# Kernel tuning notes

Measured on AMD Instinct MI355X. Metric: run time of the kernel, lower is better.

Reference implementation:

```python
import jax, jax.numpy as jnp
import numpy as np

NODE_DIM, EDGE_DIM, HIDDEN = 64, 16, 128
B, N, E, EA = 4, 10000, 320000, 80000


def _lin(key, fan_in, fan_out):
    # xavier-uniform like torch init
    bound = (6.0 / (fan_in + fan_out)) ** 0.5
    w = jax.random.uniform(key, (fan_in, fan_out), jnp.float32, -bound, bound)
    b = jnp.zeros((fan_out,), jnp.float32)
    return w, b


def setup_inputs() -> dict:
    key = jax.random.key(0)
    ks = jax.random.split(key, 12)
    nodes = jax.random.normal(ks[0], (B, N, NODE_DIM), jnp.float32)
    edge_index = jax.random.randint(ks[1], (2, E), 0, N, jnp.int64)
    edge_attr = jax.random.normal(ks[2], (B, E, EDGE_DIM), jnp.float32)
    edge_type_mask = jax.random.randint(ks[3], (EA,), 0, E, jnp.int64)
    p = {}
    p['g1_mw1'], p['g1_mb1'] = _lin(ks[4], 2 * NODE_DIM + EDGE_DIM, HIDDEN)
    p['g1_mw2'], p['g1_mb2'] = _lin(ks[5], HIDDEN, HIDDEN)
    p['g1_uw'], p['g1_ub'] = _lin(ks[6], NODE_DIM + HIDDEN, HIDDEN)
    p['g2_mw1'], p['g2_mb1'] = _lin(ks[7], 2 * HIDDEN + EDGE_DIM, HIDDEN)
    p['g2_mw2'], p['g2_mb2'] = _lin(ks[8], HIDDEN, HIDDEN)
    p['g2_uw'], p['g2_ub'] = _lin(ks[9], HIDDEN + HIDDEN, HIDDEN)
    p['a_w1'], p['a_b1'] = _lin(ks[10], 2 * HIDDEN + EDGE_DIM, HIDDEN)
    p['a_w2'], p['a_b2'] = _lin(ks[11], HIDDEN, 2)
    return dict(nodes=nodes, edge_index=edge_index, edge_attr=edge_attr,
                edge_type_mask=edge_type_mask, **p)


def _gnn_layer(node_attr, edge_index, edge_attr, mw1, mb1, mw2, mb2, uw, ub):
    r, s = edge_index[0], edge_index[1]
    h_recv = node_attr[:, r, :]          # [B,E,D] gather
    h_sent = node_attr[:, s, :]
    msg_in = jnp.concatenate([h_recv, h_sent, edge_attr], axis=-1)
    msg = jax.nn.relu(msg_in @ mw1 + mb1) @ mw2 + mb2   # [B,E,H]
    Bn, Nn, _ = node_attr.shape
    agg = jnp.zeros((Bn, Nn, msg.shape[-1]), msg.dtype).at[:, r, :].add(msg)
    upd_in = jnp.concatenate([node_attr, agg], axis=-1)
    return jax.nn.relu(upd_in @ uw + ub)


def reference(nodes, edge_index, edge_attr, edge_type_mask,
              g1_mw1, g1_mb1, g1_mw2, g1_mb2, g1_uw, g1_ub,
              g2_mw1, g2_mb1, g2_mw2, g2_mb2, g2_uw, g2_ub,
              a_w1, a_b1, a_w2, a_b2):
    h = _gnn_layer(nodes, edge_index, edge_attr, g1_mw1, g1_mb1, g1_mw2, g1_mb2, g1_uw, g1_ub)
    h = _gnn_layer(h, edge_index, edge_attr, g2_mw1, g2_mb1, g2_mw2, g2_mb2, g2_uw, g2_ub)
    # actor head: gather active edges only
    r, s = edge_index[0], edge_index[1]
    ra, sa = r[edge_type_mask], s[edge_type_mask]
    h_recv_a = h[:, ra, :]
    h_sent_a = h[:, sa, :]
    e_a = edge_attr[:, edge_type_mask, :]
    x = jnp.concatenate([h_recv_a, h_sent_a, e_a], axis=-1)
    out = jax.nn.relu(x @ a_w1 + a_b1) @ a_w2 + a_b2     # [B,EA,2]
    out = out.reshape(out.shape[0], -1, 2, out.shape[2]).mean(axis=2)  # avg edge pairs
    mean = out[:, :, 0]
    log_std = jnp.clip(out[:, :, 1], -20.0, 2.0)
    std = jnp.exp(log_std)
    return mean, std
```

## Files before the change

kernel.cpp:

```cpp
#include <hip/hip_runtime.h>
#include <hip/hip_bf16.h>
#include <math.h>

constexpr int Bn  = 4;
constexpr int Nn  = 10000;
constexpr int En  = 320000;
constexpr int EAn = 80000;
constexpr int OUT_N = 2 * Bn * (EAn / 2);

__global__ __launch_bounds__(256) void fill_sentinel(float* out, float v) {
    const int i = blockIdx.x * 256 + threadIdx.x;
    if (i < OUT_N) out[i] = v;
}

__global__ __launch_bounds__(256) void decode_indices(const void* __restrict__ ei_raw,
                                                      const void* __restrict__ mask_raw,
                                                      int* __restrict__ ei32,
                                                      int* __restrict__ mask32,
                                                      int* __restrict__ degi,
                                                      int* __restrict__ cur) {
    __shared__ int is64;
    if (threadIdx.x == 0) {
        const long long* p = (const long long*)ei_raw;
        int ok = 1;
        for (int i = 0; i < 64; i++) {
            const long long v = p[i];
            if (v < 0 || v >= (long long)Nn) { ok = 0; break; }
        }
        is64 = ok;
    }
    __syncthreads();
    const int idx    = blockIdx.x * 256 + threadIdx.x;
    const int stride = gridDim.x * 256;
    if (is64) {
        for (int i = idx; i < 2 * En; i += stride)
            ei32[i] = (int)((const long long*)ei_raw)[i];
        for (int i = idx; i < EAn; i += stride)
            mask32[i] = (int)((const long long*)mask_raw)[i];
    } else {
        for (int i = idx; i < 2 * En; i += stride)
            ei32[i] = ((const int*)ei_raw)[i];
        for (int i = idx; i < EAn; i += stride)
            mask32[i] = ((const int*)mask_raw)[i];
    }
    for (int i = idx; i < Nn; i += stride) { degi[i] = 0; cur[i] = 0; }
}

__global__ __launch_bounds__(256) void count_deg(const int* __restrict__ ei,
                                                 int* __restrict__ degi) {
    const int e = blockIdx.x * 256 + threadIdx.x;
    if (e < En) atomicAdd(&degi[ei[e]], 1);
}

__global__ __launch_bounds__(256) void scan_rowstart(const int* __restrict__ degi,
                                                     int* __restrict__ row_start) {
    __shared__ int wsum[4];
    __shared__ int carry_s;
    const int tid  = threadIdx.x;
    const int lane = tid & 63;
    const int wv   = tid >> 6;
    if (tid == 0) { carry_s = 0; row_start[0] = 0; }
    __syncthreads();
    for (int t = 0; t < 40; t++) {
        const int i = t * 256 + tid;
        int v = (i < Nn) ? degi[i] : 0;
#pragma unroll
        for (int off = 1; off < 64; off <<= 1) {
            const int x = __shfl_up(v, off);
            if (lane >= off) v += x;
        }
        if (lane == 63) wsum[wv] = v;
        __syncthreads();
        int add = 0;
        for (int w = 0; w < wv; w++) add += wsum[w];
        const int base = carry_s;
        if (i < Nn) row_start[i + 1] = base + add + v;
        __syncthreads();
        if (tid == 255) carry_s = base + add + v;
        __syncthreads();
    }
}

__global__ __launch_bounds__(256) void fill_csr(const int* __restrict__ ei,
                                                const int* __restrict__ row_start,
                                                int* __restrict__ cursor,
                                                unsigned int* __restrict__ rs_sorted,
                                                int* __restrict__ eid_sorted) {
    const int e = blockIdx.x * 256 + threadIdx.x;
    if (e < En) {
        const int r   = ei[e];
        const int s   = ei[En + e];
        const int pos = row_start[r] + atomicAdd(&cursor[r], 1);
        rs_sorted[pos]  = ((unsigned int)r << 16) | (unsigned int)s;
        eid_sorted[pos] = e;
    }
}

template <int KX>
__global__ __launch_bounds__(256) void precompute_P(const float* __restrict__ X,
                                                    const float* __restrict__ W,
                                                    float* __restrict__ P) {
    __shared__ float xs[16 * KX];
    const int m0  = blockIdx.x * 16;
    const int tid = threadIdx.x;

    for (int idx = tid * 4; idx < 16 * KX; idx += 1024)
        *(float4*)&xs[idx] = *(const float4*)&X[(size_t)m0 * KX + idx];
    __syncthreads();

    const int col  = tid;
    const int side = col >> 7;
    const int jj   = col & 127;
    const float* Wp = W + (size_t)(side * KX) * 128 + jj;

    float acc[16];
#pragma unroll
    for (int i = 0; i < 16; i++) acc[i] = 0.f;

    for (int k = 0; k < KX; k += 4) {
        const float w0 = Wp[(size_t)(k + 0) * 128];
        const float w1 = Wp[(size_t)(k + 1) * 128];
        const float w2 = Wp[(size_t)(k + 2) * 128];
        const float w3 = Wp[(size_t)(k + 3) * 128];
#pragma unroll
        for (int i = 0; i < 16; i++) {
            const float4 x = *(const float4*)&xs[i * KX + k];
            acc[i] += x.x * w0;
            acc[i] += x.y * w1;
            acc[i] += x.z * w2;
            acc[i] += x.w * w3;
        }
    }
#pragma unroll
    for (int i = 0; i < 16; i++) P[(size_t)(m0 + i) * 256 + col] = acc[i];
}

__global__ __launch_bounds__(256) void edge_scatter_sorted(const float* __restrict__ P,
                                                           const unsigned int* __restrict__ rs_sorted,
                                                           const int* __restrict__ eid_sorted,
                                                           const float* __restrict__ edge_attr,
                                                           const float* __restrict__ We,
                                                           const float* __restrict__ b1,
                                                           float* __restrict__ aggH) {
    __shared__ int   rc[32], sc[32], ec[32];
    __shared__ float eas[32 * 16];

    const int b   = blockIdx.y;
    const int e0  = blockIdx.x * 32;
    const int tid = threadIdx.x;

    if (tid < 32) {
        const unsigned int v = rs_sorted[e0 + tid];
        rc[tid] = (int)(v >> 16);
        sc[tid] = (int)(v & 0xffffu);
        ec[tid] = eid_sorted[e0 + tid];
    }
    __syncthreads();
    {
        const float* eab = edge_attr + (size_t)b * En * 16;
        if (tid < 128) {
            const int e = tid >> 2, k0 = (tid & 3) * 4;
            *(float4*)&eas[e * 16 + k0] = *(const float4*)&eab[(size_t)ec[e] * 16 + k0];
        }
    }
    __syncthreads();

    const int col  = tid & 127;
    const int half = tid >> 7;
    const int eb   = half * 16;

    float w[16];
#pragma unroll
    for (int k = 0; k < 16; k++) w[k] = We[k * 128 + col];
    const float b1c = b1[col];

    const float* Pb   = P + (size_t)b * Nn * 256;
    float*       aggb = aggH + (size_t)b * Nn * 128;

    float run  = 0.f;
    int   curR = rc[eb];
#pragma unroll 4
    for (int i = 0; i < 16; i++) {
        const int e = eb + i;
        const int r = rc[e];
        float a0 = b1c + Pb[(size_t)r * 256 + col];
        float a1 = Pb[(size_t)sc[e] * 256 + 128 + col];
        const float4 e0v = *(const float4*)&eas[e * 16 + 0];
        const float4 e1v = *(const float4*)&eas[e * 16 + 4];
        const float4 e2v = *(const float4*)&eas[e * 16 + 8];
        const float4 e3v = *(const float4*)&eas[e * 16 + 12];
        a0 += e0v.x * w[0];  a1 += e0v.y * w[1];  a0 += e0v.z * w[2];  a1 += e0v.w * w[3];
        a0 += e1v.x * w[4];  a1 += e1v.y * w[5];  a0 += e1v.z * w[6];  a1 += e1v.w * w[7];
        a0 += e2v.x * w[8];  a1 += e2v.y * w[9];  a0 += e2v.z * w[10]; a1 += e2v.w * w[11];
        a0 += e3v.x * w[12]; a1 += e3v.y * w[13]; a0 += e3v.z * w[14]; a1 += e3v.w * w[15];
        if (r != curR) {
            atomicAdd(&aggb[(size_t)curR * 128 + col], run);
            run  = 0.f;
            curR = r;
        }
        run += fmaxf(a0 + a1, 0.f);
    }
    atomicAdd(&aggb[(size_t)curR * 128 + col], run);
}

template <int KX, bool ZERO_AGG, bool WRITE_H>
__global__ __launch_bounds__(256) void fused_node_p(const float* __restrict__ X,
                                                    float* __restrict__ aggH,
                                                    const float* __restrict__ W2,
                                                    const float* __restrict__ b2,
                                                    const int* __restrict__ row_start,
                                                    const float* __restrict__ uw,
                                                    const float* __restrict__ ub,
                                                    const float* __restrict__ Wnext,
                                                    float* __restrict__ Hout,
                                                    float* __restrict__ Pout) {
    __shared__ float ah[16 * 128];
    __shared__ float ag[16 * 128];
    __shared__ float xs[16 * KX];
    __shared__ float dg[16];

    const int m0  = blockIdx.x * 16;
    const int tid = threadIdx.x;

    if (tid < 16) {
        const int row = m0 + tid;
        const int nl  = row - (row / Nn) * Nn;
        dg[tid] = (float)(row_start[nl + 1] - row_start[nl]);
    }
    for (int idx = tid * 4; idx < 16 * 128; idx += 1024)
        *(float4*)&ah[idx] = *(const float4*)&aggH[(size_t)m0 * 128 + idx];
    for (int idx = tid * 4; idx < 16 * KX; idx += 1024)
        *(float4*)&xs[idx] = *(const float4*)&X[(size_t)m0 * KX + idx];
    __syncthreads();

    if (ZERO_AGG) {
        const float4 z = {0.f, 0.f, 0.f, 0.f};
        for (int idx = tid * 4; idx < 16 * 128; idx += 1024)
            *(float4*)&aggH[(size_t)m0 * 128 + idx] = z;
    }

    const int col  = tid & 127;
    const int half = tid >> 7;

    {
        const float b2c = b2[col];
        float acc[8];
#pragma unroll
        for (int i = 0; i < 8; i++) acc[i] = dg[half * 8 + i] * b2c;
        for (int k = 0; k < 128; k += 4) {
            const float w0 = W2[(k + 0) * 128 + col];
            const float w1 = W2[(k + 1) * 128 + col];
            const float w2v = W2[(k + 2) * 128 + col];
            const float w3 = W2[(k + 3) * 128 + col];
#pragma unroll
            for (int i = 0; i < 8; i++) {
                const float4 v = *(const float4*)&ah[(half * 8 + i) * 128 + k];
                acc[i] += v.x * w0;
                acc[i] += v.y * w1;
                acc[i] += v.z * w2v;
                acc[i] += v.w * w3;
            }
        }
#pragma unroll
        for (int i = 0; i < 8; i++) ag[(half * 8 + i) * 128 + col] = acc[i];
    }
    __syncthreads();

    {
        float acc[8];
#pragma unroll
        for (int i = 0; i < 8; i++) acc[i] = ub[col];
        for (int k = 0; k < KX; k += 4) {
            const float w0 = uw[(size_t)(k + 0) * 128 + col];
            const float w1 = uw[(size_t)(k + 1) * 128 + col];
            const float w2v = uw[(size_t)(k + 2) * 128 + col];
            const float w3 = uw[(size_t)(k + 3) * 128 + col];
#pragma unroll
            for (int i = 0; i < 8; i++) {
                const float4 v = *(const float4*)&xs[(half * 8 + i) * KX + k];
                acc[i] += v.x * w0;
                acc[i] += v.y * w1;
                acc[i] += v.z * w2v;
                acc[i] += v.w * w3;
            }
        }
        for (int k = 0; k < 128; k += 4) {
            const float w0 = uw[(size_t)(KX + k + 0) * 128 + col];
            const float w1 = uw[(size_t)(KX + k + 1) * 128 + col];
            const float w2v = uw[(size_t)(KX + k + 2) * 128 + col];
            const float w3 = uw[(size_t)(KX + k + 3) * 128 + col];
#pragma unroll
            for (int i = 0; i < 8; i++) {
                const float4 v = *(const float4*)&ag[(half * 8 + i) * 128 + k];
                acc[i] += v.x * w0;
                acc[i] += v.y * w1;
                acc[i] += v.z * w2v;
                acc[i] += v.w * w3;
            }
        }
#pragma unroll
        for (int i = 0; i < 8; i++) {
            const float hv = fmaxf(acc[i], 0.f);
            ah[(half * 8 + i) * 128 + col] = hv;
            if (WRITE_H)
                Hout[(size_t)(m0 + half * 8 + i) * 128 + col] = hv;
        }
    }
    __syncthreads();

    {
        const int pcol = tid;
        const int side = pcol >> 7;
        const int jj   = pcol & 127;
        const float* Wp = Wnext + (size_t)(side * 128) * 128 + jj;
        float pacc[16];
#pragma unroll
        for (int i = 0; i < 16; i++) pacc[i] = 0.f;
        for (int k = 0; k < 128; k += 4) {
            const float w0 = Wp[(size_t)(k + 0) * 128];
            const float w1 = Wp[(size_t)(k + 1) * 128];
            const float w2v = Wp[(size_t)(k + 2) * 128];
            const float w3 = Wp[(size_t)(k + 3) * 128];
#pragma unroll
            for (int i = 0; i < 16; i++) {
                const float4 v = *(const float4*)&ah[i * 128 + k];
                pacc[i] += v.x * w0;
                pacc[i] += v.y * w1;
                pacc[i] += v.z * w2v;
                pacc[i] += v.w * w3;
            }
        }
#pragma unroll
        for (int i = 0; i < 16; i++)
            Pout[(size_t)(m0 + i) * 256 + pcol] = pacc[i];
    }
}

__global__ __launch_bounds__(256) void action_head_final(const float* __restrict__ Pa,
                                                         const int* __restrict__ ei,
                                                         const float* __restrict__ edge_attr,
                                                         const int* __restrict__ mask,
                                                         const float* __restrict__ aWe,
                                                         const float* __restrict__ b1,
                                                         const float* __restrict__ w2,
                                                         const float* __restrict__ b2,
                                                         float* __restrict__ out) {
    __shared__ int   ridx[16];
    __shared__ int   sidx[16];
    __shared__ int   eidx[16];
    __shared__ float eas[16 * 16];
    __shared__ float hid[16 * 129];
    __shared__ float o01[32];

    const int b   = blockIdx.y;
    const int j0  = blockIdx.x * 16;
    const int tid = threadIdx.x;

    if (tid < 16) {
        const int e = mask[j0 + tid];
        eidx[tid]   = e;
        ridx[tid]   = ei[e];
        sidx[tid]   = ei[En + e];
    }
    __syncthreads();
    if (tid < 64) {
        const float* eab = edge_attr + (size_t)b * En * 16;
        const int e = tid >> 2, k0 = (tid & 3) * 4;
        *(float4*)&eas[e * 16 + k0] = *(const float4*)&eab[(size_t)eidx[e] * 16 + k0];
    }
    __syncthreads();

    const int col  = tid & 127;
    const int half = tid >> 7;
    float w[16];
#pragma unroll
    for (int k = 0; k < 16; k++) w[k] = aWe[k * 128 + col];
    const float b1c = b1[col];
    const float* Pab = Pa + (size_t)b * Nn * 256;

#pragma unroll
    for (int i = 0; i < 8; i++) {
        const int e = half * 8 + i;
        float a0 = b1c + Pab[(size_t)ridx[e] * 256 + col];
        float a1 = Pab[(size_t)sidx[e] * 256 + 128 + col];
        const float4 e0v = *(const float4*)&eas[e * 16 + 0];
        const float4 e1v = *(const float4*)&eas[e * 16 + 4];
        const float4 e2v = *(const float4*)&eas[e * 16 + 8];
        const float4 e3v = *(const float4*)&eas[e * 16 + 12];
        a0 += e0v.x * w[0];  a1 += e0v.y * w[1];  a0 += e0v.z * w[2];  a1 += e0v.w * w[3];
        a0 += e1v.x * w[4];  a1 += e1v.y * w[5];  a0 += e1v.z * w[6];  a1 += e1v.w * w[7];
        a0 += e2v.x * w[8];  a1 += e2v.y * w[9];  a0 += e2v.z * w[10]; a1 += e2v.w * w[11];
        a0 += e3v.x * w[12]; a1 += e3v.y * w[13]; a0 += e3v.z * w[14]; a1 += e3v.w * w[15];
        hid[e * 129 + col] = fmaxf(a0 + a1, 0.f);
    }
    __syncthreads();

    const int g    = tid >> 4;
    const int lane = tid & 15;
    float o0 = 0.f, o1 = 0.f;
#pragma unroll
    for (int k = lane; k < 128; k += 16) {
        const float hv = hid[g * 129 + k];
        o0 += hv * w2[k * 2 + 0];
        o1 += hv * w2[k * 2 + 1];
    }
#pragma unroll
    for (int m = 8; m >= 1; m >>= 1) {
        o0 += __shfl_xor(o0, m);
        o1 += __shfl_xor(o1, m);
    }
    if (lane == 0) {
        o01[g * 2 + 0] = o0 + b2[0];
        o01[g * 2 + 1] = o1 + b2[1];
    }
    __syncthreads();

    if (tid < 8) {
        const float mean = 0.5f * (o01[4 * tid + 0] + o01[4 * tid + 2]);
        float l          = 0.5f * (o01[4 * tid + 1] + o01[4 * tid + 3]);
        l = fminf(fmaxf(l, -20.f), 2.f);
        constexpr int HALF = EAn / 2;
        const int idx = b * HALF + j0 / 2 + tid;
        out[idx]             = mean;
        out[Bn * HALF + idx] = expf(l);
    }
}

extern "C" void kernel_launch(void* const* d_in, const int* in_sizes, int n_in,
                              void* d_out, int out_size, void* d_ws, size_t ws_size,
                              hipStream_t stream) {
    (void)out_size;

    static const long long want[20] = {
        (long long)Bn * Nn * 64, 2LL * En, (long long)Bn * En * 16, (long long)EAn,
        144 * 128, 128, 128 * 128, 128, 192 * 128, 128,
        272 * 128, 128, 128 * 128, 128, 256 * 128, 128,
        272 * 128, 128, 128 * 2, 2};
    bool sig_ok = (n_in == 20);
    if (sig_ok)
        for (int i = 0; i < 20; i++) sig_ok = sig_ok && (in_sizes[i] == want[i]);

    const size_t PF   = (size_t)Bn * Nn * 256;
    const size_t aggF = (size_t)Bn * Nn * 128;
    const size_t hF   = (size_t)Bn * Nn * 128;
    const size_t needWords = PF + aggF + hF + 2 * En + EAn + (Nn + 16) + En + En;
    const size_t needBytes = needWords * 4;

    const dim3 blk(256);
    if (!sig_ok) {
        fill_sentinel<<<(OUT_N + 255) / 256, blk, 0, stream>>>((float*)d_out, 5555.f);
        return;
    }
    if (ws_size < needBytes) {
        fill_sentinel<<<(OUT_N + 255) / 256, blk, 0, stream>>>((float*)d_out, 9999.f);
        return;
    }

    const float* nodes  = (const float*)d_in[0];
    const void*  ei_raw = d_in[1];
    const float* eattr  = (const float*)d_in[2];
    const void*  mk_raw = d_in[3];
    const float* g1_mw1 = (const float*)d_in[4];
    const float* g1_mb1 = (const float*)d_in[5];
    const float* g1_mw2 = (const float*)d_in[6];
    const float* g1_mb2 = (const float*)d_in[7];
    const float* g1_uw  = (const float*)d_in[8];
    const float* g1_ub  = (const float*)d_in[9];
    const float* g2_mw1 = (const float*)d_in[10];
    const float* g2_mb1 = (const float*)d_in[11];
    const float* g2_mw2 = (const float*)d_in[12];
    const float* g2_mb2 = (const float*)d_in[13];
    const float* g2_uw  = (const float*)d_in[14];
    const float* g2_ub  = (const float*)d_in[15];
    const float* a_w1   = (const float*)d_in[16];
    const float* a_b1   = (const float*)d_in[17];
    const float* a_w2   = (const float*)d_in[18];
    const float* a_b2   = (const float*)d_in[19];

    float*        P     = (float*)d_ws;
    float*        aggH  = P + PF;
    float*        h     = aggH + aggF;
    int*          ei32  = (int*)(h + hF);
    int*          mk32  = ei32 + 2 * En;
    int*          rowst = mk32 + EAn;
    unsigned int* rsS   = (unsigned int*)(rowst + (Nn + 16));
    int*          eidS  = (int*)(rsS + En);
    int*   degi = (int*)h;
    int*   cur  = degi + Nn;

    const int  nbNodes = (Bn * Nn) / 16;
    const dim3 gEdge(En / 32, Bn);
    const dim3 gAct(EAn / 16, Bn);
    const size_t aggBytes = aggF * 4;

    decode_indices<<<2500, blk, 0, stream>>>(ei_raw, mk_raw, ei32, mk32, degi, cur);
    count_deg<<<En / 256, blk, 0, stream>>>(ei32, degi);
    scan_rowstart<<<1, blk, 0, stream>>>(degi, rowst);
    fill_csr<<<En / 256, blk, 0, stream>>>(ei32, rowst, cur, rsS, eidS);

    precompute_P<64><<<nbNodes, blk, 0, stream>>>(nodes, g1_mw1, P);
    hipMemsetAsync(aggH, 0, aggBytes, stream);
    edge_scatter_sorted<<<gEdge, blk, 0, stream>>>(P, rsS, eidS, eattr,
                                                   g1_mw1 + 128 * 128, g1_mb1, aggH);
    fused_node_p<64, true, true><<<nbNodes, blk, 0, stream>>>(
        nodes, aggH, g1_mw2, g1_mb2, rowst, g1_uw, g1_ub, g2_mw1, h, P);

    edge_scatter_sorted<<<gEdge, blk, 0, stream>>>(P, rsS, eidS, eattr,
                                                   g2_mw1 + 256 * 128, g2_mb1, aggH);
    fused_node_p<128, false, false><<<nbNodes, blk, 0, stream>>>(
        h, aggH, g2_mw2, g2_mb2, rowst, g2_uw, g2_ub, a_w1, nullptr, P);

    action_head_final<<<gAct, blk, 0, stream>>>(P, ei32, eattr, mk32,
                                                a_w1 + 256 * 128, a_b1,
                                                a_w2, a_b2, (float*)d_out);
}
```

Before: 759.5 us.

## Loop batches inside edge scatter kernel and reuse receiver row loads

The edge scatter kernel now handles all four batches in one block instead of one batch per grid row. Edge indices, weights and bias are therefore loaded once per block and reused across batches, and the edge attributes for every batch are staged in shared memory up front. The receiver-side P value is loaded only when the receiver changes, since edges are sorted by receiver. In exchange the grid is four times smaller, with more serial work per block and more shared memory per block, which may reduce parallelism and latency hiding.

```diff
diff --git a/kernel.cpp b/kernel.cpp
--- a/kernel.cpp
+++ b/kernel.cpp
@@ -143,9 +143,8 @@
                                                            const float* __restrict__ b1,
                                                            float* __restrict__ aggH) {
     __shared__ int   rc[32], sc[32], ec[32];
-    __shared__ float eas[32 * 16];
-
-    const int b   = blockIdx.y;
+    __shared__ float eas[4][32 * 16];
+
     const int e0  = blockIdx.x * 32;
     const int tid = threadIdx.x;
 
@@ -156,12 +155,12 @@
         ec[tid] = eid_sorted[e0 + tid];
     }
     __syncthreads();
-    {
-        const float* eab = edge_attr + (size_t)b * En * 16;
-        if (tid < 128) {
-            const int e = tid >> 2, k0 = (tid & 3) * 4;
-            *(float4*)&eas[e * 16 + k0] = *(const float4*)&eab[(size_t)ec[e] * 16 + k0];
-        }
+    for (int t = tid; t < 512; t += 256) {
+        const int bb = t >> 7;
+        const int e  = (t >> 2) & 31;
+        const int k0 = (t & 3) * 4;
+        *(float4*)&eas[bb][e * 16 + k0] =
+            *(const float4*)&edge_attr[(((size_t)bb * En + ec[e]) * 16) + k0];
     }
     __syncthreads();
 
@@ -174,33 +173,38 @@
     for (int k = 0; k < 16; k++) w[k] = We[k * 128 + col];
     const float b1c = b1[col];
 
-    const float* Pb   = P + (size_t)b * Nn * 256;
-    float*       aggb = aggH + (size_t)b * Nn * 128;
-
-    float run  = 0.f;
-    int   curR = rc[eb];
+    for (int b = 0; b < Bn; b++) {
+        const float* Pb   = P + (size_t)b * Nn * 256;
+        float*       aggb = aggH + (size_t)b * Nn * 128;
+        const float* easb = eas[b];
+
+        int   curR = rc[eb];
+        float prv  = b1c + Pb[(size_t)curR * 256 + col];
+        float run  = 0.f;
 #pragma unroll 4
-    for (int i = 0; i < 16; i++) {
-        const int e = eb + i;
-        const int r = rc[e];
-        float a0 = b1c + Pb[(size_t)r * 256 + col];
-        float a1 = Pb[(size_t)sc[e] * 256 + 128 + col];
-        const float4 e0v = *(const float4*)&eas[e * 16 + 0];
-        const float4 e1v = *(const float4*)&eas[e * 16 + 4];
-        const float4 e2v = *(const float4*)&eas[e * 16 + 8];
-        const float4 e3v = *(const float4*)&eas[e * 16 + 12];
-        a0 += e0v.x * w[0];  a1 += e0v.y * w[1];  a0 += e0v.z * w[2];  a1 += e0v.w * w[3];
-        a0 += e1v.x * w[4];  a1 += e1v.y * w[5];  a0 += e1v.z * w[6];  a1 += e1v.w * w[7];
-        a0 += e2v.x * w[8];  a1 += e2v.y * w[9];  a0 += e2v.z * w[10]; a1 += e2v.w * w[11];
-        a0 += e3v.x * w[12]; a1 += e3v.y * w[13]; a0 += e3v.z * w[14]; a1 += e3v.w * w[15];
-        if (r != curR) {
-            atomicAdd(&aggb[(size_t)curR * 128 + col], run);
-            run  = 0.f;
-            curR = r;
-        }
-        run += fmaxf(a0 + a1, 0.f);
-    }
-    atomicAdd(&aggb[(size_t)curR * 128 + col], run);
+        for (int i = 0; i < 16; i++) {
+            const int e = eb + i;
+            const int r = rc[e];
+            if (r != curR) {
+                atomicAdd(&aggb[(size_t)curR * 128 + col], run);
+                run  = 0.f;
+                curR = r;
+                prv  = b1c + Pb[(size_t)r * 256 + col];
+            }
+            float a0 = prv;
+            float a1 = Pb[(size_t)sc[e] * 256 + 128 + col];
+            const float4 e0v = *(const float4*)&easb[e * 16 + 0];
+            const float4 e1v = *(const float4*)&easb[e * 16 + 4];
+            const float4 e2v = *(const float4*)&easb[e * 16 + 8];
+            const float4 e3v = *(const float4*)&easb[e * 16 + 12];
+            a0 += e0v.x * w[0];  a1 += e0v.y * w[1];  a0 += e0v.z * w[2];  a1 += e0v.w * w[3];
+            a0 += e1v.x * w[4];  a1 += e1v.y * w[5];  a0 += e1v.z * w[6];  a1 += e1v.w * w[7];
+            a0 += e2v.x * w[8];  a1 += e2v.y * w[9];  a0 += e2v.z * w[10]; a1 += e2v.w * w[11];
+            a0 += e3v.x * w[12]; a1 += e3v.y * w[13]; a0 += e3v.z * w[14]; a1 += e3v.w * w[15];
+            run += fmaxf(a0 + a1, 0.f);
+        }
+        atomicAdd(&aggb[(size_t)curR * 128 + col], run);
+    }
 }
 
 template <int KX, bool ZERO_AGG, bool WRITE_H>
@@ -489,7 +493,7 @@
     int*   cur  = degi + Nn;
 
     const int  nbNodes = (Bn * Nn) / 16;
-    const dim3 gEdge(En / 32, Bn);
+    const dim3 gEdge(En / 32, 1);
     const dim3 gAct(EAn / 16, Bn);
     const size_t aggBytes = aggF * 4;
 
```

Measured after the change: 787.0 us. 1.04x slower.
